# Performance work log

Measured on AMD Instinct MI355X. Metric: run time of the kernel, lower is better.

## Reference

```python
import jax, jax.numpy as jnp
import numpy as np

EPSILON = 1e-10
T, N, IN_DIM = 50, 2048, 16   # seq_len, num_stocks, lstm input dims
R, K, H = 8, 32, 128          # relations, max neighbors, lstm hidden dims


def setup_inputs() -> dict:
    key = jax.random.key(0)
    ks = jax.random.split(key, 10)
    s = 1.0 / np.sqrt(H)
    stock_hist = jax.random.normal(ks[0], (T, N, IN_DIM), dtype=jnp.float32)
    neighbors = jax.random.randint(ks[1], (R, N, K), 0, N + 1, dtype=jnp.int32)
    # rel_num: count of real (nonzero) neighbors per relation per stock
    rel_num = jnp.sum(neighbors != 0, axis=-1).astype(jnp.float32)  # [R, N]
    return {
        "stock_hist": stock_hist,
        "neighbors": neighbors,
        "rel_num": rel_num,
        # LSTM params (torch gate order i,f,g,o)
        "W_ih": jax.random.normal(ks[2], (4 * H, IN_DIM), dtype=jnp.float32) * s,
        "W_hh": jax.random.normal(ks[3], (4 * H, H), dtype=jnp.float32) * s,
        "b_ih": jnp.zeros((4 * H,), dtype=jnp.float32),
        "b_hh": jnp.zeros((4 * H,), dtype=jnp.float32),
        # fc_att: Linear(2H + R -> 1)
        "w_att": jax.random.normal(ks[4], (2 * H + R,), dtype=jnp.float32) * s,
        "b_att": jnp.zeros((), dtype=jnp.float32),
        # fc_rel_att: Linear(H + R -> 1)
        "w_rel": jax.random.normal(ks[5], (H + R,), dtype=jnp.float32) * s,
        "b_rel": jnp.zeros((), dtype=jnp.float32),
        "w_fc1": jax.random.normal(ks[6], (H, 1), dtype=jnp.float32) * s,
        "b_fc1": jnp.zeros((1,), dtype=jnp.float32),
    }


def _lstm_final_h(x, W_ih, W_hh, b_ih, b_hh):
    # x: [T, N, In] -> final hidden state h_T: [N, H]
    n = x.shape[1]
    h0 = jnp.zeros((n, H), x.dtype)
    c0 = jnp.zeros((n, H), x.dtype)

    def step(carry, x_t):
        h, c = carry
        z = x_t @ W_ih.T + h @ W_hh.T + (b_ih + b_hh)
        i, f, g, o = jnp.split(z, 4, axis=-1)
        c = jax.nn.sigmoid(f) * c + jax.nn.sigmoid(i) * jnp.tanh(g)
        h = jax.nn.sigmoid(o) * jnp.tanh(c)
        return (h, c), None

    (h, _), _ = jax.lax.scan(step, (h0, c0), x)
    return h


def reference(stock_hist, neighbors, rel_num, W_ih, W_hh, b_ih, b_hh,
              w_att, b_att, w_rel, b_rel, w_fc1, b_fc1):
    se = _lstm_final_h(stock_hist, W_ih, W_hh, b_ih, b_hh)        # [N, H]
    se_pad = jnp.concatenate([jnp.zeros((1, H), se.dtype), se], 0)  # row 0 = padding

    # --- graph attention layer ---
    nb_emb = se_pad[neighbors]                                    # [R, N, K, H] gather
    # fc_att over concat(nb_emb, self_emb, one_hot(R)) == split-weight matvecs
    w_nb, w_self, w_oh = w_att[:H], w_att[H:2 * H], w_att[2 * H:]
    score = (nb_emb @ w_nb                                        # [R, N, K]
             + (se @ w_self)[None, :, None]                       # self emb broadcast
             + w_oh[:, None, None]                                # one-hot relation emb
             + b_att)
    att_w = jax.nn.softmax(score, axis=2)                         # softmax over neighbors
    rel_rep = jnp.einsum('rnk,rnkh->rnh', att_w, nb_emb) / (rel_num + EPSILON)[..., None]

    # fc_rel_att over concat(rel_rep, one_hot(R))
    wr_h, wr_oh = w_rel[:H], w_rel[H:]
    rscore = rel_rep @ wr_h + wr_oh[:, None] + b_rel              # [R, N]
    rel_w = jax.nn.softmax(rscore, axis=0)                        # softmax over relations
    updated = jnp.mean(rel_w[..., None] * rel_rep, axis=0)        # [N, H]

    final = updated + se                                          # residual (state_embedding[1:])
    preds = final @ w_fc1 + b_fc1
    return preds
```

## Files before the change

kernel.cpp:

```cpp
#include <hip/hip_runtime.h>
#include <math.h>

#define T_STEPS 50
#define NS      2048
#define IND     16
#define HID     128
#define GATES   512
#define RR      8
#define KN      32
#define EPSV    1e-10f

#define LROWS   8
#define LTH     512
#define XPAD    20

#define LOG2E      1.44269504f
#define TWO_LOG2E  2.88539008f

typedef _Float16 f16x8 __attribute__((ext_vector_type(8)));
typedef _Float16 f16x4 __attribute__((ext_vector_type(4)));
typedef float    f32x4 __attribute__((ext_vector_type(4)));

__device__ __forceinline__ float rcp_(float x)  { return __builtin_amdgcn_rcpf(x); }
__device__ __forceinline__ float sigm2(float zt) {
    return rcp_(1.0f + __builtin_amdgcn_exp2f(zt));
}
__device__ __forceinline__ float tanh2(float zt) {
    return 1.0f - 2.0f * rcp_(1.0f + __builtin_amdgcn_exp2f(zt));
}

__global__ __launch_bounds__(LTH, 2) void lstm_mfma_kernel(
    const float* __restrict__ x,
    const float* __restrict__ W_ih,
    const float* __restrict__ W_hh,
    const float* __restrict__ b_ih,
    const float* __restrict__ b_hh,
    const float* __restrict__ w_att,
    float* __restrict__ se,
    _Float16* __restrict__ se16,
    float* __restrict__ sw,
    float* __restrict__ p2n)
{
    __shared__ __align__(16) _Float16 sA[2][16][HID];
    __shared__ __align__(16) _Float16 sX[T_STEPS][16][XPAD];
    __shared__ float spart[8][4][4];

    const int tid    = threadIdx.x;
    const int w      = tid >> 6;
    const int l      = tid & 63;
    const int lane16 = l & 15;
    const int lgrp   = l >> 4;
    const int n0     = blockIdx.x * LROWS;

    f16x8 Bh[4][4];
    f16x4 Bx[4];
    f32x4 bias4[4];
#pragma unroll
    for (int gg = 0; gg < 4; ++gg) {
        const float sc = (gg == 2) ? TWO_LOG2E : -LOG2E;
        const int gi = 128 * gg + 16 * w + lane16;
        const float bv = sc * (b_ih[gi] + b_hh[gi]);
        bias4[gg] = (f32x4){bv, bv, bv, bv};
        const float4 wx = *(const float4*)&W_ih[gi * IND + lgrp * 4];
        f16x4 vx = { (_Float16)(sc * wx.x), (_Float16)(sc * wx.y),
                     (_Float16)(sc * wx.z), (_Float16)(sc * wx.w) };
        Bx[gg] = vx;
#pragma unroll
        for (int kf = 0; kf < 4; ++kf) {
            const float4* p4 = (const float4*)(W_hh + gi * HID + kf * 32 + lgrp * 8);
            const float4 a = p4[0], b = p4[1];
            f16x8 v = { (_Float16)(sc * a.x), (_Float16)(sc * a.y),
                        (_Float16)(sc * a.z), (_Float16)(sc * a.w),
                        (_Float16)(sc * b.x), (_Float16)(sc * b.y),
                        (_Float16)(sc * b.z), (_Float16)(sc * b.w) };
            Bh[gg][kf] = v;
        }
    }
#pragma unroll
    for (int gg = 0; gg < 4; ++gg) {
        asm volatile("" : "+v"(Bx[gg]));
        asm volatile("" : "+v"(bias4[gg]));
#pragma unroll
        for (int kf = 0; kf < 4; ++kf)
            asm volatile("" : "+v"(Bh[gg][kf]));
    }

    for (int i = tid; i < 2 * 16 * HID; i += LTH)
        (&sA[0][0][0])[i] = (_Float16)0.0f;
    for (int i = tid; i < T_STEPS * 16 * XPAD; i += LTH)
        (&sX[0][0][0])[i] = (_Float16)0.0f;
    __syncthreads();

    for (int i = tid; i < T_STEPS * LROWS * IND; i += LTH) {
        const int t = i >> 7, e = i & 127;
        sX[t][2 * (e >> 4)][e & 15] = (_Float16)x[((size_t)t * NS + n0) * IND + e];
    }
    __syncthreads();

    const int axor  = (lane16 & 7) << 4;
    const int abase = lane16 * (HID * 2);
    const int hrow0 = 4 * lgrp, hrow1 = 4 * lgrp + 2;
    const int hcol2 = (16 * w + lane16) * 2;
    const int hb0   = hrow0 * (HID * 2) + (hcol2 ^ ((hrow0 & 7) << 4));
    const int hb1   = hrow1 * (HID * 2) + (hcol2 ^ ((hrow1 & 7) << 4));

    float c0 = 0.f, c1 = 0.f, h0 = 0.f, h1 = 0.f;

    f32x4 azx0, azx1, azx2, azx3;
    {
        f16x4 Ax = *(const f16x4*)&sX[0][lane16][lgrp * 4];
        azx0 = __builtin_amdgcn_mfma_f32_16x16x16f16(Ax, Bx[0], bias4[0], 0, 0, 0);
        azx1 = __builtin_amdgcn_mfma_f32_16x16x16f16(Ax, Bx[1], bias4[1], 0, 0, 0);
        azx2 = __builtin_amdgcn_mfma_f32_16x16x16f16(Ax, Bx[2], bias4[2], 0, 0, 0);
        azx3 = __builtin_amdgcn_mfma_f32_16x16x16f16(Ax, Bx[3], bias4[3], 0, 0, 0);
    }

    for (int step = 0; step < T_STEPS; ++step) {
        const int cur = step & 1;
        const char* ab = (const char*)&sA[cur][0][0] + abase;

        f16x8 Ah[4];
#pragma unroll
        for (int kf = 0; kf < 4; ++kf)
            Ah[kf] = *(const f16x8*)(ab + ((kf * 64 + lgrp * 16) ^ axor));

        f32x4 az0 = azx0, az1 = azx1, az2 = azx2, az3 = azx3;
#pragma unroll
        for (int kf = 0; kf < 4; ++kf) {
            az0 = __builtin_amdgcn_mfma_f32_16x16x32_f16(Ah[kf], Bh[0][kf], az0, 0, 0, 0);
            az1 = __builtin_amdgcn_mfma_f32_16x16x32_f16(Ah[kf], Bh[1][kf], az1, 0, 0, 0);
            az2 = __builtin_amdgcn_mfma_f32_16x16x32_f16(Ah[kf], Bh[2][kf], az2, 0, 0, 0);
            az3 = __builtin_amdgcn_mfma_f32_16x16x32_f16(Ah[kf], Bh[3][kf], az3, 0, 0, 0);
        }

        {
            const int nstep = (step + 1 < T_STEPS) ? step + 1 : step;
            f16x4 Ax = *(const f16x4*)&sX[nstep][lane16][lgrp * 4];
            azx0 = __builtin_amdgcn_mfma_f32_16x16x16f16(Ax, Bx[0], bias4[0], 0, 0, 0);
            azx1 = __builtin_amdgcn_mfma_f32_16x16x16f16(Ax, Bx[1], bias4[1], 0, 0, 0);
            azx2 = __builtin_amdgcn_mfma_f32_16x16x16f16(Ax, Bx[2], bias4[2], 0, 0, 0);
            azx3 = __builtin_amdgcn_mfma_f32_16x16x16f16(Ax, Bx[3], bias4[3], 0, 0, 0);
        }

        char* wb = (char*)&sA[cur ^ 1][0][0];

        c0 = sigm2(az1[0]) * c0 + sigm2(az0[0]) * tanh2(az2[0]);
        h0 = sigm2(az3[0]) * tanh2(TWO_LOG2E * c0);
        if (step + 1 < T_STEPS)
            *(_Float16*)(wb + hb0) = (_Float16)h0;

        c1 = sigm2(az1[2]) * c1 + sigm2(az0[2]) * tanh2(az2[2]);
        h1 = sigm2(az3[2]) * tanh2(TWO_LOG2E * c1);
        if (step + 1 < T_STEPS)
            *(_Float16*)(wb + hb1) = (_Float16)h1;

        __syncthreads();
    }

    const int col = 16 * w + lane16;
    se[(n0 + 2 * lgrp) * HID + col]       = h0;
    se[(n0 + 2 * lgrp + 1) * HID + col]   = h1;
    se16[(n0 + 2 * lgrp) * HID + col]     = (_Float16)h0;
    se16[(n0 + 2 * lgrp + 1) * HID + col] = (_Float16)h1;

    float d0 = h0 * w_att[col];
    float d1 = h1 * w_att[col];
    float d2 = h0 * w_att[HID + col];
    float d3 = h1 * w_att[HID + col];
#pragma unroll
    for (int m = 8; m > 0; m >>= 1) {
        d0 += __shfl_xor(d0, m);
        d1 += __shfl_xor(d1, m);
        d2 += __shfl_xor(d2, m);
        d3 += __shfl_xor(d3, m);
    }
    if (lane16 == 0) {
        spart[w][lgrp][0] = d0;
        spart[w][lgrp][1] = d1;
        spart[w][lgrp][2] = d2;
        spart[w][lgrp][3] = d3;
    }
    __syncthreads();
    if (tid < 16) {
        const int r8 = tid >> 1;
        const int q  = tid & 1;
        const int lg = r8 >> 1, o = r8 & 1;
        float v = 0.f;
#pragma unroll
        for (int ww = 0; ww < 8; ++ww)
            v += spart[ww][lg][o + 2 * q];
        if (q == 0) sw[n0 + r8] = v;
        else        p2n[n0 + r8] = v;
    }
}

__global__ __launch_bounds__(512) void attn_fused_kernel(
    const _Float16* __restrict__ se16,
    const float* __restrict__ se,
    const int*   __restrict__ neighbors,
    const float* __restrict__ rel_num,
    const float* __restrict__ sw,
    const float* __restrict__ p2n,
    const float* __restrict__ w_att,
    const float* __restrict__ b_att,
    const float* __restrict__ w_rel,
    const float* __restrict__ b_rel,
    const float* __restrict__ w_fc1,
    const float* __restrict__ b_fc1,
    float* __restrict__ out)
{
    __shared__ float srel[RR][HID];
    __shared__ float srsc[RR];

    const int r    = threadIdx.x >> 6;
    const int lane = threadIdx.x & 63;
    const int n    = blockIdx.x;
    const size_t pair = (size_t)r * NS + n;

    int myidx = 0;
    if (lane < KN) myidx = neighbors[pair * KN + lane];

    float s = 0.f;
    if (lane < KN) {
        float swv = (myidx != 0) ? sw[myidx - 1] : 0.f;
        s = swv + p2n[n] + w_att[2 * HID + r] + b_att[0];
    }
    float mx = s;
#pragma unroll
    for (int d = 16; d > 0; d >>= 1) mx = fmaxf(mx, __shfl_xor(mx, d, 32));
    float e  = __expf(s - mx);
    float sm = e;
#pragma unroll
    for (int d = 16; d > 0; d >>= 1) sm += __shfl_xor(sm, d, 32);
    float att = e * rcp_(sm);

    const int q  = lane >> 4;
    const int c8 = lane & 15;
    const f16x8* se16_8 = (const f16x8*)se16;
    float acc[8];
#pragma unroll
    for (int j = 0; j < 8; ++j) acc[j] = 0.f;
#pragma unroll
    for (int kk = 0; kk < KN / 4; ++kk) {
        const int   kq = kk * 4 + q;
        const float av = __shfl(att, kq);
        const int  idq = __shfl(myidx, kq);
        if (idq != 0) {
            f16x8 v = se16_8[(size_t)(idq - 1) * 16 + c8];
#pragma unroll
            for (int j = 0; j < 8; ++j) acc[j] += av * (float)v[j];
        }
    }
#pragma unroll
    for (int j = 0; j < 8; ++j) {
        acc[j] += __shfl_xor(acc[j], 16);
        acc[j] += __shfl_xor(acc[j], 32);
    }

    const float inv = rcp_(rel_num[pair] + EPSV);
    float pr = 0.f;
    if (q == 0) {
#pragma unroll
        for (int j = 0; j < 8; ++j) acc[j] *= inv;
        float4 w0 = make_float4(acc[0], acc[1], acc[2], acc[3]);
        float4 w1 = make_float4(acc[4], acc[5], acc[6], acc[7]);
        *(float4*)&srel[r][c8 * 8]     = w0;
        *(float4*)&srel[r][c8 * 8 + 4] = w1;
#pragma unroll
        for (int j = 0; j < 8; ++j) pr += acc[j] * w_rel[c8 * 8 + j];
    }
#pragma unroll
    for (int d = 8; d > 0; d >>= 1) pr += __shfl_xor(pr, d, 16);
    if (lane == 0) srsc[r] = pr + w_rel[HID + r] + b_rel[0];

    __syncthreads();

    if (r == 0) {
        float rs[RR];
        float rmx = -1e30f;
#pragma unroll
        for (int qq = 0; qq < RR; ++qq) {
            rs[qq] = srsc[qq];
            rmx = fmaxf(rmx, rs[qq]);
        }
        float rsm = 0.f;
#pragma unroll
        for (int qq = 0; qq < RR; ++qq) {
            rs[qq] = __expf(rs[qq] - rmx);
            rsm += rs[qq];
        }
        const float invs = rcp_(rsm * (float)RR);

        float u0 = 0.f, u1 = 0.f;
#pragma unroll
        for (int qq = 0; qq < RR; ++qq) {
            u0 += rs[qq] * srel[qq][lane];
            u1 += rs[qq] * srel[qq][64 + lane];
        }
        u0 = u0 * invs + se[n * HID + lane];
        u1 = u1 * invs + se[n * HID + 64 + lane];

        float p = u0 * w_fc1[lane] + u1 * w_fc1[64 + lane];
#pragma unroll
        for (int d = 32; d > 0; d >>= 1) p += __shfl_xor(p, d);
        if (lane == 0) out[n] = p + b_fc1[0];
    }
}

extern "C" void kernel_launch(void* const* d_in, const int* in_sizes, int n_in,
                              void* d_out, int out_size, void* d_ws, size_t ws_size,
                              hipStream_t stream) {
    const float* x      = (const float*)d_in[0];
    const int*   nbrs   = (const int*)  d_in[1];
    const float* relnum = (const float*)d_in[2];
    const float* W_ih   = (const float*)d_in[3];
    const float* W_hh   = (const float*)d_in[4];
    const float* b_ih   = (const float*)d_in[5];
    const float* b_hh   = (const float*)d_in[6];
    const float* w_att  = (const float*)d_in[7];
    const float* b_att  = (const float*)d_in[8];
    const float* w_rel  = (const float*)d_in[9];
    const float* b_rel  = (const float*)d_in[10];
    const float* w_fc1  = (const float*)d_in[11];
    const float* b_fc1  = (const float*)d_in[12];
    float* out = (float*)d_out;

    float*    se   = (float*)d_ws;
    _Float16* se16 = (_Float16*)(se + (size_t)NS * HID);
    float*    sw   = (float*)(se16 + (size_t)NS * HID);
    float*    p2n  = sw + NS;

    hipLaunchKernelGGL(lstm_mfma_kernel, dim3(NS / LROWS), dim3(LTH), 0, stream,
                       x, W_ih, W_hh, b_ih, b_hh, w_att, se, se16, sw, p2n);
    hipLaunchKernelGGL(attn_fused_kernel, dim3(NS), dim3(512), 0, stream,
                       se16, se, nbrs, relnum, sw, p2n, w_att, b_att,
                       w_rel, b_rel, w_fc1, b_fc1, out);
}
```

Baseline: 57.70 us.

## Remap attention kernel to one wave per stock, looping over relations

The attention kernel used to give each block one stock and each wave one relation, so the eight relation scores had to be combined through shared memory and a block barrier. Now each wave handles one stock and loops over all eight relations, keeping the relation scores in registers and removing __syncthreads. The grid shrinks from 2048 blocks to 256, and the softmax exponentials switch to exp2f. Per-wave serial work grows and there are fewer waves in flight to hide gather latency, while the LSTM kernel, which likely dominates total time, is unchanged.

Result: slower. 67.75 us (+17.4%).

```diff
diff --git a/kernel.cpp b/kernel.cpp
--- a/kernel.cpp
+++ b/kernel.cpp
@@ -209,102 +209,100 @@
     const float* __restrict__ b_fc1,
     float* __restrict__ out)
 {
-    __shared__ float srel[RR][HID];
-    __shared__ float srsc[RR];
-
-    const int r    = threadIdx.x >> 6;
+    __shared__ float srel[8][RR][HID];
+
+    const int wv   = threadIdx.x >> 6;
     const int lane = threadIdx.x & 63;
-    const int n    = blockIdx.x;
-    const size_t pair = (size_t)r * NS + n;
-
-    int myidx = 0;
-    if (lane < KN) myidx = neighbors[pair * KN + lane];
-
-    float s = 0.f;
-    if (lane < KN) {
-        float swv = (myidx != 0) ? sw[myidx - 1] : 0.f;
-        s = swv + p2n[n] + w_att[2 * HID + r] + b_att[0];
-    }
-    float mx = s;
-#pragma unroll
-    for (int d = 16; d > 0; d >>= 1) mx = fmaxf(mx, __shfl_xor(mx, d, 32));
-    float e  = __expf(s - mx);
-    float sm = e;
-#pragma unroll
-    for (int d = 16; d > 0; d >>= 1) sm += __shfl_xor(sm, d, 32);
-    float att = e * rcp_(sm);
-
+    const int n    = blockIdx.x * 8 + wv;
+
+    const f16x8* se16_8 = (const f16x8*)se16;
     const int q  = lane >> 4;
     const int c8 = lane & 15;
-    const f16x8* se16_8 = (const f16x8*)se16;
-    float acc[8];
-#pragma unroll
-    for (int j = 0; j < 8; ++j) acc[j] = 0.f;
-#pragma unroll
-    for (int kk = 0; kk < KN / 4; ++kk) {
-        const int   kq = kk * 4 + q;
-        const float av = __shfl(att, kq);
-        const int  idq = __shfl(myidx, kq);
-        if (idq != 0) {
-            f16x8 v = se16_8[(size_t)(idq - 1) * 16 + c8];
-#pragma unroll
-            for (int j = 0; j < 8; ++j) acc[j] += av * (float)v[j];
-        }
-    }
-#pragma unroll
-    for (int j = 0; j < 8; ++j) {
-        acc[j] += __shfl_xor(acc[j], 16);
-        acc[j] += __shfl_xor(acc[j], 32);
-    }
-
-    const float inv = rcp_(rel_num[pair] + EPSV);
-    float pr = 0.f;
-    if (q == 0) {
-#pragma unroll
-        for (int j = 0; j < 8; ++j) acc[j] *= inv;
-        float4 w0 = make_float4(acc[0], acc[1], acc[2], acc[3]);
-        float4 w1 = make_float4(acc[4], acc[5], acc[6], acc[7]);
-        *(float4*)&srel[r][c8 * 8]     = w0;
-        *(float4*)&srel[r][c8 * 8 + 4] = w1;
-#pragma unroll
-        for (int j = 0; j < 8; ++j) pr += acc[j] * w_rel[c8 * 8 + j];
-    }
-#pragma unroll
-    for (int d = 8; d > 0; d >>= 1) pr += __shfl_xor(pr, d, 16);
-    if (lane == 0) srsc[r] = pr + w_rel[HID + r] + b_rel[0];
-
-    __syncthreads();
-
-    if (r == 0) {
-        float rs[RR];
-        float rmx = -1e30f;
-#pragma unroll
-        for (int qq = 0; qq < RR; ++qq) {
-            rs[qq] = srsc[qq];
-            rmx = fmaxf(rmx, rs[qq]);
-        }
-        float rsm = 0.f;
-#pragma unroll
-        for (int qq = 0; qq < RR; ++qq) {
-            rs[qq] = __expf(rs[qq] - rmx);
-            rsm += rs[qq];
-        }
-        const float invs = rcp_(rsm * (float)RR);
-
-        float u0 = 0.f, u1 = 0.f;
-#pragma unroll
-        for (int qq = 0; qq < RR; ++qq) {
-            u0 += rs[qq] * srel[qq][lane];
-            u1 += rs[qq] * srel[qq][64 + lane];
-        }
-        u0 = u0 * invs + se[n * HID + lane];
-        u1 = u1 * invs + se[n * HID + 64 + lane];
-
-        float p = u0 * w_fc1[lane] + u1 * w_fc1[64 + lane];
-#pragma unroll
-        for (int d = 32; d > 0; d >>= 1) p += __shfl_xor(p, d);
-        if (lane == 0) out[n] = p + b_fc1[0];
-    }
+    const float p2v  = p2n[n];
+    const float batt = b_att[0];
+
+    float rsc[RR];
+
+#pragma unroll
+    for (int r = 0; r < RR; ++r) {
+        const size_t pair = (size_t)r * NS + n;
+
+        int myidx = 0;
+        if (lane < KN) myidx = neighbors[pair * KN + lane];
+
+        float s = 0.f;
+        if (lane < KN) {
+            float swv = (myidx != 0) ? sw[myidx - 1] : 0.f;
+            s = swv + p2v + w_att[2 * HID + r] + batt;
+        }
+        float mx = s;
+#pragma unroll
+        for (int d = 16; d > 0; d >>= 1) mx = fmaxf(mx, __shfl_xor(mx, d, 32));
+        float e  = __builtin_amdgcn_exp2f(LOG2E * (s - mx));
+        float sm = e;
+#pragma unroll
+        for (int d = 16; d > 0; d >>= 1) sm += __shfl_xor(sm, d, 32);
+        const float att = e * rcp_(sm);
+
+        float acc[8];
+#pragma unroll
+        for (int j = 0; j < 8; ++j) acc[j] = 0.f;
+#pragma unroll
+        for (int kk = 0; kk < KN / 4; ++kk) {
+            const int   kq = kk * 4 + q;
+            const float av = __shfl(att, kq);
+            const int  idq = __shfl(myidx, kq);
+            if (idq != 0) {
+                f16x8 v = se16_8[(size_t)(idq - 1) * 16 + c8];
+#pragma unroll
+                for (int j = 0; j < 8; ++j) acc[j] += av * (float)v[j];
+            }
+        }
+#pragma unroll
+        for (int j = 0; j < 8; ++j) {
+            acc[j] += __shfl_xor(acc[j], 16);
+            acc[j] += __shfl_xor(acc[j], 32);
+        }
+
+        const float inv = rcp_(rel_num[pair] + EPSV);
+        float pr = 0.f;
+        if (q == 0) {
+#pragma unroll
+            for (int j = 0; j < 8; ++j) acc[j] *= inv;
+            *(float4*)&srel[wv][r][c8 * 8]     = make_float4(acc[0], acc[1], acc[2], acc[3]);
+            *(float4*)&srel[wv][r][c8 * 8 + 4] = make_float4(acc[4], acc[5], acc[6], acc[7]);
+#pragma unroll
+            for (int j = 0; j < 8; ++j) pr += acc[j] * w_rel[c8 * 8 + j];
+        }
+#pragma unroll
+        for (int d = 8; d > 0; d >>= 1) pr += __shfl_xor(pr, d, 16);
+        rsc[r] = __shfl(pr, 0) + w_rel[HID + r] + b_rel[0];
+    }
+
+    float rmx = -1e30f;
+#pragma unroll
+    for (int r = 0; r < RR; ++r) rmx = fmaxf(rmx, rsc[r]);
+    float rsm = 0.f;
+#pragma unroll
+    for (int r = 0; r < RR; ++r) {
+        rsc[r] = __builtin_amdgcn_exp2f(LOG2E * (rsc[r] - rmx));
+        rsm += rsc[r];
+    }
+    const float invs = rcp_(rsm * (float)RR);
+
+    float u0 = 0.f, u1 = 0.f;
+#pragma unroll
+    for (int r = 0; r < RR; ++r) {
+        u0 += rsc[r] * srel[wv][r][lane];
+        u1 += rsc[r] * srel[wv][r][64 + lane];
+    }
+    u0 = u0 * invs + se[n * HID + lane];
+    u1 = u1 * invs + se[n * HID + 64 + lane];
+
+    float p = u0 * w_fc1[lane] + u1 * w_fc1[64 + lane];
+#pragma unroll
+    for (int d = 32; d > 0; d >>= 1) p += __shfl_xor(p, d);
+    if (lane == 0) out[n] = p + b_fc1[0];
 }
 
 extern "C" void kernel_launch(void* const* d_in, const int* in_sizes, int n_in,
@@ -332,7 +330,7 @@
 
     hipLaunchKernelGGL(lstm_mfma_kernel, dim3(NS / LROWS), dim3(LTH), 0, stream,
                        x, W_ih, W_hh, b_ih, b_hh, w_att, se, se16, sw, p2n);
-    hipLaunchKernelGGL(attn_fused_kernel, dim3(NS), dim3(512), 0, stream,
+    hipLaunchKernelGGL(attn_fused_kernel, dim3(NS / 8), dim3(512), 0, stream,
                        se16, se, nbrs, relnum, sw, p2n, w_att, b_att,
                        w_rel, b_rel, w_fc1, b_fc1, out);
 }
```
